# Kernel optimization log

Measured on AMD Instinct MI355X. Metric: run time of the kernel, lower is better.

Reference implementation:

```python
import jax, jax.numpy as jnp
import numpy as np

B, T, D, H, E = 4, 2048, 1024, 2048, 8
TOP_K = int(E * 0.25)  # = 2


def setup_inputs() -> dict:
    key = jax.random.key(0)
    ks = jax.random.split(key, 6)
    x = jax.random.normal(ks[0], (B, T, D), dtype=jnp.float32)
    gate = jax.random.normal(ks[1], (D, E), dtype=jnp.float32)
    # per-expert 2-layer MLP params (D -> H -> D), stacked over experts
    W1 = jax.random.normal(ks[2], (E, D, H), dtype=jnp.float32) * (D ** -0.5)
    b1 = jnp.zeros((E, H), dtype=jnp.float32)
    W2 = jax.random.normal(ks[3], (E, H, D), dtype=jnp.float32) * (H ** -0.5)
    b2 = jnp.zeros((E, D), dtype=jnp.float32)
    return {"x": x, "gate": gate, "W1": W1, "b1": b1, "W2": W2, "b2": b2}


def reference(x, gate, W1, b1, W2, b2):
    # gating: softmax over experts, then top-k mask, renormalize (L1 over experts)
    raw_gate = jax.nn.softmax(jnp.einsum('btd,de->bte', x, gate), axis=-1)  # [B,T,E]
    topk_scores, topk_idx = jax.lax.top_k(raw_gate, TOP_K)                   # [B,T,k]
    mask = jax.nn.one_hot(topk_idx, E, dtype=raw_gate.dtype).sum(axis=-2)    # [B,T,E]
    gate_topk = mask * raw_gate
    gate_topk = gate_topk / jnp.maximum(gate_topk.sum(axis=-1, keepdims=True), 1e-12)
    # dense all-expert compute (faithful to the original: every expert sees every token)
    h = jax.nn.relu(jnp.einsum('btd,edh->beth', x, W1) + b1[None, :, None, :])  # [B,E,T,H]
    expert_out = jnp.einsum('beth,ehd->betd', h, W2) + b2[None, :, None, :]     # [B,E,T,D]
    # weighted combine
    out = jnp.einsum('bte,betd->btd', gate_topk, expert_out)  # [B,T,D]
    return out
```

## Files before the change

### kernel.cpp

```cpp
#include <hip/hip_runtime.h>

#define E_      8
#define D_      1024
#define H_      2048
#define TOKENS  8192
#define RROWS   16384
#define HPAD_ROWS (RROWS + 128)

using bf16x8 = __attribute__((ext_vector_type(8))) __bf16;
using f32x4  = __attribute__((ext_vector_type(4))) float;

__device__ __forceinline__ unsigned short f2bf(float f) {
  unsigned u = __builtin_bit_cast(unsigned, f);
  u += 0x7fffu + ((u >> 16) & 1u);
  return (unsigned short)(u >> 16);
}
__device__ __forceinline__ float bf2f(unsigned short u) {
  unsigned v = (unsigned)u << 16;
  return __builtin_bit_cast(float, v);
}

#define GLDS16(g, l) __builtin_amdgcn_global_load_lds( \
    (const __attribute__((address_space(1))) unsigned int*)(g), \
    (__attribute__((address_space(3))) unsigned int*)(l), 16, 0, 0)

#define SBAR() asm volatile("s_barrier" ::: "memory")


__global__ void transpose_cvt_kernel(const float* __restrict__ src,
                                     unsigned short* __restrict__ dst,
                                     int R, int C) {
  int tilesC = C >> 6, tilesR = R >> 6;
  int per = tilesR * tilesC;
  int b = blockIdx.x;
  int e = b / per, rem = b % per;
  int rb = rem / tilesC, cb = rem % tilesC;
  __shared__ float tile[64][65];
  const float* s = src + (size_t)e * R * C;
  unsigned short* d = dst + (size_t)e * R * C;
  int r0 = rb << 6, c0 = cb << 6;
#pragma unroll
  for (int i = 0; i < 16; i++) {
    int idx = threadIdx.x + i * 256;
    int lr = idx >> 6, lc = idx & 63;
    tile[lr][lc] = s[(size_t)(r0 + lr) * C + (c0 + lc)];
  }
  __syncthreads();
#pragma unroll
  for (int i = 0; i < 16; i++) {
    int idx = threadIdx.x + i * 256;
    int lr = idx >> 6, lc = idx & 63;
    d[(size_t)(c0 + lr) * R + (r0 + lc)] = f2bf(tile[lc][lr]);
  }
}

__global__ void gating_kernel(const float* __restrict__ x, const float* __restrict__ gate,
                              unsigned short* __restrict__ xb,
                              int* __restrict__ sel, float* __restrict__ wsel) {
  int lane = threadIdx.x & 63, wid = threadIdx.x >> 6;
  int t = (blockIdx.x << 2) + wid;
  const float* xr = x + (size_t)t * D_;
  unsigned short* xbr = xb + (size_t)t * D_;
  float acc[8];
#pragma unroll
  for (int e = 0; e < 8; e++) acc[e] = 0.f;
#pragma unroll
  for (int i = 0; i < 4; i++) {
    int d0 = (i << 8) + (lane << 2);
    float4 xv = *reinterpret_cast<const float4*>(xr + d0);
    ushort4 o = make_ushort4(f2bf(xv.x), f2bf(xv.y), f2bf(xv.z), f2bf(xv.w));
    *reinterpret_cast<ushort4*>(xbr + d0) = o;
    float xa[4] = {xv.x, xv.y, xv.z, xv.w};
#pragma unroll
    for (int j = 0; j < 4; j++) {
      const float4* g4 = reinterpret_cast<const float4*>(gate + (size_t)(d0 + j) * 8);
      float4 ga = g4[0], gb = g4[1];
      acc[0] += xa[j] * ga.x; acc[1] += xa[j] * ga.y;
      acc[2] += xa[j] * ga.z; acc[3] += xa[j] * ga.w;
      acc[4] += xa[j] * gb.x; acc[5] += xa[j] * gb.y;
      acc[6] += xa[j] * gb.z; acc[7] += xa[j] * gb.w;
    }
  }
#pragma unroll
  for (int e = 0; e < 8; e++) {
#pragma unroll
    for (int off = 32; off; off >>= 1) acc[e] += __shfl_xor(acc[e], off);
  }
  if (lane == 0) {
    int i0 = 0; float v0 = acc[0];
#pragma unroll
    for (int e = 1; e < 8; e++) if (acc[e] > v0) { v0 = acc[e]; i0 = e; }
    int i1 = -1; float v1 = -3.4e38f;
#pragma unroll
    for (int e = 0; e < 8; e++) if (e != i0 && acc[e] > v1) { v1 = acc[e]; i1 = e; }
    float p1 = expf(v1 - v0);
    float inv = 1.f / (1.f + p1);
    sel[t * 2] = i0; sel[t * 2 + 1] = i1;
    wsel[t * 2] = inv; wsel[t * 2 + 1] = p1 * inv;
  }
}

__global__ __launch_bounds__(1024) void route_kernel(
    const int* __restrict__ sel, int* __restrict__ cnt, int* __restrict__ off,
    int* __restrict__ tok_id, int* __restrict__ pos) {
  const int tid = threadIdx.x;
  const int lane = tid & 63, wid = tid >> 6;
  __shared__ int wtot[16][8];
  __shared__ int woff[16][8];
  __shared__ int offs[8];
  int sv[16];
  const int s0 = tid << 4;
#pragma unroll
  for (int q = 0; q < 4; q++) {
    int4 v = reinterpret_cast<const int4*>(sel + s0)[q];
    sv[q * 4 + 0] = v.x; sv[q * 4 + 1] = v.y;
    sv[q * 4 + 2] = v.z; sv[q * 4 + 3] = v.w;
  }
  int h[8];
#pragma unroll
  for (int e = 0; e < 8; e++) h[e] = 0;
#pragma unroll
  for (int j = 0; j < 16; j++) {
    int ev = sv[j];
#pragma unroll
    for (int e = 0; e < 8; e++) h[e] += (ev == e) ? 1 : 0;
  }
  int excl[8];
#pragma unroll
  for (int e = 0; e < 8; e++) {
    int v = h[e];
#pragma unroll
    for (int d = 1; d < 64; d <<= 1) {
      int u = __shfl_up(v, d);
      if (lane >= d) v += u;
    }
    excl[e] = v - h[e];
    if (lane == 63) wtot[wid][e] = v;
  }
  __syncthreads();
  if (tid == 0) {
    int run[8];
#pragma unroll
    for (int e = 0; e < 8; e++) run[e] = 0;
    for (int w = 0; w < 16; w++)
#pragma unroll
      for (int e = 0; e < 8; e++) { woff[w][e] = run[e]; run[e] += wtot[w][e]; }
    int a = 0;
    for (int e = 0; e < 8; e++) { offs[e] = a; off[e] = a; cnt[e] = run[e]; a += run[e]; }
  }
  __syncthreads();
  int base[8];
#pragma unroll
  for (int e = 0; e < 8; e++) base[e] = offs[e] + woff[wid][e] + excl[e];
#pragma unroll
  for (int j = 0; j < 16; j++) {
    int ev = sv[j];
    int p = 0;
#pragma unroll
    for (int e = 0; e < 8; e++) if (ev == e) { p = base[e]; base[e] = p + 1; }
    pos[s0 + j] = p;
    tok_id[p] = (s0 + j) >> 1;
  }
}


#define STAGE_T(slot, kh) do { \
  const size_t ko = (size_t)(kh) << 7; \
  _Pragma("unroll") \
  for (int i = 0; i < 4; i++) { \
    GLDS16(Ab + gA[i] + ko, &Asm[slot][((wid << 2) + i) << 9]); \
    GLDS16(Bb + gB[i] + ko, &Bsm[slot][((wid << 2) + i) << 9]); \
  } \
} while (0)

__global__ __launch_bounds__(256, 2) void gemm1_kernel(
    const unsigned short* __restrict__ xb,
    const unsigned short* __restrict__ w1t,
    const float* __restrict__ b1,
    unsigned short* __restrict__ hbuf,
    const int* __restrict__ tok_id,
    const int* __restrict__ cnt, const int* __restrict__ off) {
  const int nwg = E_ * 64 * 16;
  const int raw = blockIdx.x;
  const int bid = (raw & 7) * (nwg >> 3) + (raw >> 3);
  const int e  = bid >> 10;
  const int rb = (bid >> 4) & 63;
  const int cb = bid & 15;
  const int rows = cnt[e];
  const int m0 = rb << 7;
  if (m0 >= rows) return;
  const int base = off[e];
  const int tid = threadIdx.x, lane = tid & 63, wid = tid >> 6;
  const int wr = wid >> 1, wc = wid & 1;

  __shared__ __align__(16) unsigned short Asm[2][128 * 64];
  __shared__ __align__(16) unsigned short Bsm[2][128 * 64];

  const int c8 = lane & 7, r8 = lane >> 3;
  const size_t swz = (size_t)((c8 ^ r8) << 4);
  size_t gA[4], gB[4];
  const int n0 = cb << 7;
#pragma unroll
  for (int i = 0; i < 4; i++) {
    int r = ((wid << 2) + i) << 3;
    int ar = m0 + r + r8; if (ar >= rows) ar = rows - 1;
    gA[i] = (size_t)tok_id[base + ar] * (D_ * 2) + swz;
    gB[i] = (size_t)(n0 + r + r8) * (D_ * 2) + swz;
  }
  const char* Ab = (const char*)xb;
  const char* Bb = (const char*)w1t + (size_t)e * H_ * D_ * 2;

  const int aRow = ((wr << 6) + (lane & 15)) * 128;
  const int bRow = ((wc << 6) + (lane & 15)) * 128;
  const int cby0 = (((lane >> 4)) ^ (lane & 7)) << 4;
  const int cby1 = ((4 + (lane >> 4)) ^ (lane & 7)) << 4;

  f32x4 acc[4][4] = {};
  const int KH = D_ / 64;

  STAGE_T(0, 0);
  STAGE_T(1, 1);
  asm volatile("s_waitcnt vmcnt(8)" ::: "memory");
  SBAR();

  for (int kh = 0; kh < KH; ++kh) {
    const int cur = kh & 1;
    const char* Ap = (const char*)&Asm[cur][0] + aRow;
    const char* Bp = (const char*)&Bsm[cur][0] + bRow;
    bf16x8 a[4], b[4], a2[4], b2[4];
#pragma unroll
    for (int m = 0; m < 4; m++) a[m]  = *(const bf16x8*)(Ap + cby0 + m * 2048);
#pragma unroll
    for (int n = 0; n < 4; n++) b[n]  = *(const bf16x8*)(Bp + cby0 + n * 2048);
#pragma unroll
    for (int m = 0; m < 4; m++) a2[m] = *(const bf16x8*)(Ap + cby1 + m * 2048);
#pragma unroll
    for (int n = 0; n < 4; n++) b2[n] = *(const bf16x8*)(Bp + cby1 + n * 2048);
    asm volatile("s_waitcnt lgkmcnt(0)" ::: "memory");
    __builtin_amdgcn_sched_barrier(0);
    SBAR();
    if (kh + 2 < KH) STAGE_T(cur, kh + 2);
    __builtin_amdgcn_s_setprio(1);
#pragma unroll
    for (int m = 0; m < 4; m++)
#pragma unroll
      for (int n = 0; n < 4; n++)
        acc[m][n] = __builtin_amdgcn_mfma_f32_16x16x32_bf16(a[m], b[n], acc[m][n], 0, 0, 0);
#pragma unroll
    for (int m = 0; m < 4; m++)
#pragma unroll
      for (int n = 0; n < 4; n++)
        acc[m][n] = __builtin_amdgcn_mfma_f32_16x16x32_bf16(a2[m], b2[n], acc[m][n], 0, 0, 0);
    __builtin_amdgcn_s_setprio(0);
    if (kh + 2 < KH) {
      asm volatile("s_waitcnt vmcnt(8)" ::: "memory");
    } else if (kh + 1 < KH) {
      asm volatile("s_waitcnt vmcnt(0)" ::: "memory");
    }
    SBAR();
  }

  const int rcnt = rows - m0;
  const float* b1e = b1 + e * H_;
#pragma unroll
  for (int m = 0; m < 4; m++) {
#pragma unroll
    for (int q = 0; q < 4; q++) {
      int rl = (wr << 6) + (m << 4) + ((lane >> 4) << 2) + q;
      if (rl < rcnt) {
        unsigned short* hrow = hbuf + (size_t)(base + m0 + rl) * H_;
#pragma unroll
        for (int n = 0; n < 4; n++) {
          int ncol = n0 + (wc << 6) + (n << 4) + (lane & 15);
          float v = acc[m][n][q] + b1e[ncol];
          hrow[ncol] = f2bf(fmaxf(v, 0.f));
        }
      }
    }
  }
}

__global__ __launch_bounds__(256, 2) void gemm2_kernel(
    const unsigned short* __restrict__ hbuf,
    const unsigned short* __restrict__ w2t,
    unsigned short* __restrict__ eout,
    const int* __restrict__ cnt, const int* __restrict__ off) {
  const int nwg = E_ * 64 * 8;
  const int raw = blockIdx.x;
  const int bid = (raw & 7) * (nwg >> 3) + (raw >> 3);
  const int e  = bid >> 9;
  const int rb = (bid >> 3) & 63;
  const int cb = bid & 7;
  const int rows = cnt[e];
  const int m0 = rb << 7;
  if (m0 >= rows) return;
  const int base = off[e];
  const int tid = threadIdx.x, lane = tid & 63, wid = tid >> 6;
  const int wr = wid >> 1, wc = wid & 1;

  __shared__ __align__(16) unsigned short Asm[2][128 * 64];
  __shared__ __align__(16) unsigned short Bsm[2][128 * 64];

  const int c8 = lane & 7, r8 = lane >> 3;
  const size_t swz = (size_t)((c8 ^ r8) << 4);
  size_t gA[4], gB[4];
  const int n0 = cb << 7;
#pragma unroll
  for (int i = 0; i < 4; i++) {
    int r = ((wid << 2) + i) << 3;
    gA[i] = (size_t)(base + m0 + r + r8) * (H_ * 2) + swz;
    gB[i] = (size_t)(n0 + r + r8) * (H_ * 2) + swz;
  }
  const char* Ab = (const char*)hbuf;
  const char* Bb = (const char*)w2t + (size_t)e * D_ * H_ * 2;

  const int aRow = ((wr << 6) + (lane & 15)) * 128;
  const int bRow = ((wc << 6) + (lane & 15)) * 128;
  const int cby0 = (((lane >> 4)) ^ (lane & 7)) << 4;
  const int cby1 = ((4 + (lane >> 4)) ^ (lane & 7)) << 4;

  f32x4 acc[4][4] = {};
  const int KH = H_ / 64;

  STAGE_T(0, 0);
  STAGE_T(1, 1);
  asm volatile("s_waitcnt vmcnt(8)" ::: "memory");
  SBAR();

  for (int kh = 0; kh < KH; ++kh) {
    const int cur = kh & 1;
    const char* Ap = (const char*)&Asm[cur][0] + aRow;
    const char* Bp = (const char*)&Bsm[cur][0] + bRow;
    bf16x8 a[4], b[4], a2[4], b2[4];
#pragma unroll
    for (int m = 0; m < 4; m++) a[m]  = *(const bf16x8*)(Ap + cby0 + m * 2048);
#pragma unroll
    for (int n = 0; n < 4; n++) b[n]  = *(const bf16x8*)(Bp + cby0 + n * 2048);
#pragma unroll
    for (int m = 0; m < 4; m++) a2[m] = *(const bf16x8*)(Ap + cby1 + m * 2048);
#pragma unroll
    for (int n = 0; n < 4; n++) b2[n] = *(const bf16x8*)(Bp + cby1 + n * 2048);
    asm volatile("s_waitcnt lgkmcnt(0)" ::: "memory");
    __builtin_amdgcn_sched_barrier(0);
    SBAR();
    if (kh + 2 < KH) STAGE_T(cur, kh + 2);
    __builtin_amdgcn_s_setprio(1);
#pragma unroll
    for (int m = 0; m < 4; m++)
#pragma unroll
      for (int n = 0; n < 4; n++)
        acc[m][n] = __builtin_amdgcn_mfma_f32_16x16x32_bf16(a[m], b[n], acc[m][n], 0, 0, 0);
#pragma unroll
    for (int m = 0; m < 4; m++)
#pragma unroll
      for (int n = 0; n < 4; n++)
        acc[m][n] = __builtin_amdgcn_mfma_f32_16x16x32_bf16(a2[m], b2[n], acc[m][n], 0, 0, 0);
    __builtin_amdgcn_s_setprio(0);
    if (kh + 2 < KH) {
      asm volatile("s_waitcnt vmcnt(8)" ::: "memory");
    } else if (kh + 1 < KH) {
      asm volatile("s_waitcnt vmcnt(0)" ::: "memory");
    }
    SBAR();
  }

  const int rcnt = rows - m0;
#pragma unroll
  for (int m = 0; m < 4; m++) {
#pragma unroll
    for (int q = 0; q < 4; q++) {
      int rl = (wr << 6) + (m << 4) + ((lane >> 4) << 2) + q;
      if (rl < rcnt) {
        unsigned short* erow = eout + (size_t)(base + m0 + rl) * D_;
#pragma unroll
        for (int n = 0; n < 4; n++) {
          int ncol = n0 + (wc << 6) + (n << 4) + (lane & 15);
          erow[ncol] = f2bf(acc[m][n][q]);
        }
      }
    }
  }
}

__global__ void combine_kernel(const unsigned short* __restrict__ eout,
                               const float* __restrict__ b2,
                               const int* __restrict__ sel, const float* __restrict__ wsel,
                               const int* __restrict__ pos,
                               float* __restrict__ out) {
  int t = blockIdx.x;
  int d = threadIdx.x << 2;
  int e0 = sel[t * 2], e1 = sel[t * 2 + 1];
  float w0 = wsel[t * 2], w1 = wsel[t * 2 + 1];
  int p0 = pos[t * 2], p1 = pos[t * 2 + 1];
  ushort4 y0 = *reinterpret_cast<const ushort4*>(eout + (size_t)p0 * D_ + d);
  ushort4 y1 = *reinterpret_cast<const ushort4*>(eout + (size_t)p1 * D_ + d);
  float4 c0 = *reinterpret_cast<const float4*>(b2 + (size_t)e0 * D_ + d);
  float4 c1 = *reinterpret_cast<const float4*>(b2 + (size_t)e1 * D_ + d);
  float4 o;
  o.x = w0 * (bf2f(y0.x) + c0.x) + w1 * (bf2f(y1.x) + c1.x);
  o.y = w0 * (bf2f(y0.y) + c0.y) + w1 * (bf2f(y1.y) + c1.y);
  o.z = w0 * (bf2f(y0.z) + c0.z) + w1 * (bf2f(y1.z) + c1.z);
  o.w = w0 * (bf2f(y0.w) + c0.w) + w1 * (bf2f(y1.w) + c1.w);
  *reinterpret_cast<float4*>(out + (size_t)t * D_ + d) = o;
}


extern "C" void kernel_launch(void* const* d_in, const int* in_sizes, int n_in,
                              void* d_out, int out_size, void* d_ws, size_t ws_size,
                              hipStream_t stream) {
  (void)in_sizes; (void)n_in; (void)ws_size; (void)out_size;
  const float* x    = (const float*)d_in[0];
  const float* gate = (const float*)d_in[1];
  const float* W1   = (const float*)d_in[2];
  const float* b1   = (const float*)d_in[3];
  const float* W2   = (const float*)d_in[4];
  const float* b2   = (const float*)d_in[5];
  float* out = (float*)d_out;

  char* p = (char*)d_ws;
  unsigned short* xb   = (unsigned short*)p; p += (size_t)TOKENS * D_ * 2;
  unsigned short* w1t  = (unsigned short*)p; p += (size_t)E_ * H_ * D_ * 2;
  unsigned short* w2t  = (unsigned short*)p; p += (size_t)E_ * D_ * H_ * 2;
  unsigned short* hbuf = (unsigned short*)p; p += (size_t)HPAD_ROWS * H_ * 2;
  int*   tok  = (int*)p;   p += (size_t)RROWS * 4;
  int*   pos  = (int*)p;   p += (size_t)TOKENS * 2 * 4;
  int*   sel  = (int*)p;   p += (size_t)TOKENS * 2 * 4;
  float* wsel = (float*)p; p += (size_t)TOKENS * 2 * 4;
  int* cnt    = (int*)p;   p += 32 * 4;
  int* off    = (int*)p;   p += 32 * 4;
  unsigned short* eout = w1t;

  transpose_cvt_kernel<<<E_ * (D_ / 64) * (H_ / 64), 256, 0, stream>>>(W1, w1t, D_, H_);
  transpose_cvt_kernel<<<E_ * (H_ / 64) * (D_ / 64), 256, 0, stream>>>(W2, w2t, H_, D_);
  gating_kernel<<<TOKENS / 4, 256, 0, stream>>>(x, gate, xb, sel, wsel);
  route_kernel<<<1, 1024, 0, stream>>>(sel, cnt, off, tok, pos);
  gemm1_kernel<<<E_ * 64 * 16, 256, 0, stream>>>(xb, w1t, b1, hbuf, tok, cnt, off);
  gemm2_kernel<<<E_ * 64 * 8, 256, 0, stream>>>(hbuf, w2t, eout, cnt, off);
  combine_kernel<<<TOKENS, 256, 0, stream>>>(eout, b2, sel, wsel, pos, out);
}
```

Before: 299.1 us.

## Enlarge grouped GEMM tiles to 256x256 with 512-thread workgroups

Both expert GEMMs move from 128x128 output tiles with 4 waves to 256x256 tiles with 8 waves. Each wave now holds a 128x64 accumulator block and interleaves the two half-K MFMA passes with LDS fragment loads. The goal is more reuse per byte staged into LDS and fewer workgroups. In exchange it uses 128KB of LDS per block and many more accumulator registers, and it adds padding waste on ragged per-expert row counts, which is why the hbuf padding is increased.

```diff
diff --git a/kernel.cpp b/kernel.cpp
--- a/kernel.cpp
+++ b/kernel.cpp
@@ -5,7 +5,7 @@
 #define H_      2048
 #define TOKENS  8192
 #define RROWS   16384
-#define HPAD_ROWS (RROWS + 128)
+#define HPAD_ROWS (RROWS + 256)
 
 using bf16x8 = __attribute__((ext_vector_type(8))) __bf16;
 using f32x4  = __attribute__((ext_vector_type(4))) float;
@@ -164,126 +164,21 @@
 }
 
 
-#define STAGE_T(slot, kh) do { \
+#define STAGE256(slot, kh) do { \
   const size_t ko = (size_t)(kh) << 7; \
   _Pragma("unroll") \
   for (int i = 0; i < 4; i++) { \
-    GLDS16(Ab + gA[i] + ko, &Asm[slot][((wid << 2) + i) << 9]); \
-    GLDS16(Bb + gB[i] + ko, &Bsm[slot][((wid << 2) + i) << 9]); \
+    GLDS16(Ab + aO[i] + ko, (char*)&Asm[slot][0] + (i << 13) + (wid << 10)); \
+    GLDS16(Bb + bO[i] + ko, (char*)&Bsm[slot][0] + (i << 13) + (wid << 10)); \
   } \
 } while (0)
 
-__global__ __launch_bounds__(256, 2) void gemm1_kernel(
+__global__ __launch_bounds__(512, 2) void gemm1_kernel(
     const unsigned short* __restrict__ xb,
     const unsigned short* __restrict__ w1t,
     const float* __restrict__ b1,
     unsigned short* __restrict__ hbuf,
     const int* __restrict__ tok_id,
-    const int* __restrict__ cnt, const int* __restrict__ off) {
-  const int nwg = E_ * 64 * 16;
-  const int raw = blockIdx.x;
-  const int bid = (raw & 7) * (nwg >> 3) + (raw >> 3);
-  const int e  = bid >> 10;
-  const int rb = (bid >> 4) & 63;
-  const int cb = bid & 15;
-  const int rows = cnt[e];
-  const int m0 = rb << 7;
-  if (m0 >= rows) return;
-  const int base = off[e];
-  const int tid = threadIdx.x, lane = tid & 63, wid = tid >> 6;
-  const int wr = wid >> 1, wc = wid & 1;
-
-  __shared__ __align__(16) unsigned short Asm[2][128 * 64];
-  __shared__ __align__(16) unsigned short Bsm[2][128 * 64];
-
-  const int c8 = lane & 7, r8 = lane >> 3;
-  const size_t swz = (size_t)((c8 ^ r8) << 4);
-  size_t gA[4], gB[4];
-  const int n0 = cb << 7;
-#pragma unroll
-  for (int i = 0; i < 4; i++) {
-    int r = ((wid << 2) + i) << 3;
-    int ar = m0 + r + r8; if (ar >= rows) ar = rows - 1;
-    gA[i] = (size_t)tok_id[base + ar] * (D_ * 2) + swz;
-    gB[i] = (size_t)(n0 + r + r8) * (D_ * 2) + swz;
-  }
-  const char* Ab = (const char*)xb;
-  const char* Bb = (const char*)w1t + (size_t)e * H_ * D_ * 2;
-
-  const int aRow = ((wr << 6) + (lane & 15)) * 128;
-  const int bRow = ((wc << 6) + (lane & 15)) * 128;
-  const int cby0 = (((lane >> 4)) ^ (lane & 7)) << 4;
-  const int cby1 = ((4 + (lane >> 4)) ^ (lane & 7)) << 4;
-
-  f32x4 acc[4][4] = {};
-  const int KH = D_ / 64;
-
-  STAGE_T(0, 0);
-  STAGE_T(1, 1);
-  asm volatile("s_waitcnt vmcnt(8)" ::: "memory");
-  SBAR();
-
-  for (int kh = 0; kh < KH; ++kh) {
-    const int cur = kh & 1;
-    const char* Ap = (const char*)&Asm[cur][0] + aRow;
-    const char* Bp = (const char*)&Bsm[cur][0] + bRow;
-    bf16x8 a[4], b[4], a2[4], b2[4];
-#pragma unroll
-    for (int m = 0; m < 4; m++) a[m]  = *(const bf16x8*)(Ap + cby0 + m * 2048);
-#pragma unroll
-    for (int n = 0; n < 4; n++) b[n]  = *(const bf16x8*)(Bp + cby0 + n * 2048);
-#pragma unroll
-    for (int m = 0; m < 4; m++) a2[m] = *(const bf16x8*)(Ap + cby1 + m * 2048);
-#pragma unroll
-    for (int n = 0; n < 4; n++) b2[n] = *(const bf16x8*)(Bp + cby1 + n * 2048);
-    asm volatile("s_waitcnt lgkmcnt(0)" ::: "memory");
-    __builtin_amdgcn_sched_barrier(0);
-    SBAR();
-    if (kh + 2 < KH) STAGE_T(cur, kh + 2);
-    __builtin_amdgcn_s_setprio(1);
-#pragma unroll
-    for (int m = 0; m < 4; m++)
-#pragma unroll
-      for (int n = 0; n < 4; n++)
-        acc[m][n] = __builtin_amdgcn_mfma_f32_16x16x32_bf16(a[m], b[n], acc[m][n], 0, 0, 0);
-#pragma unroll
-    for (int m = 0; m < 4; m++)
-#pragma unroll
-      for (int n = 0; n < 4; n++)
-        acc[m][n] = __builtin_amdgcn_mfma_f32_16x16x32_bf16(a2[m], b2[n], acc[m][n], 0, 0, 0);
-    __builtin_amdgcn_s_setprio(0);
-    if (kh + 2 < KH) {
-      asm volatile("s_waitcnt vmcnt(8)" ::: "memory");
-    } else if (kh + 1 < KH) {
-      asm volatile("s_waitcnt vmcnt(0)" ::: "memory");
-    }
-    SBAR();
-  }
-
-  const int rcnt = rows - m0;
-  const float* b1e = b1 + e * H_;
-#pragma unroll
-  for (int m = 0; m < 4; m++) {
-#pragma unroll
-    for (int q = 0; q < 4; q++) {
-      int rl = (wr << 6) + (m << 4) + ((lane >> 4) << 2) + q;
-      if (rl < rcnt) {
-        unsigned short* hrow = hbuf + (size_t)(base + m0 + rl) * H_;
-#pragma unroll
-        for (int n = 0; n < 4; n++) {
-          int ncol = n0 + (wc << 6) + (n << 4) + (lane & 15);
-          float v = acc[m][n][q] + b1e[ncol];
-          hrow[ncol] = f2bf(fmaxf(v, 0.f));
-        }
-      }
-    }
-  }
-}
-
-__global__ __launch_bounds__(256, 2) void gemm2_kernel(
-    const unsigned short* __restrict__ hbuf,
-    const unsigned short* __restrict__ w2t,
-    unsigned short* __restrict__ eout,
     const int* __restrict__ cnt, const int* __restrict__ off) {
   const int nwg = E_ * 64 * 8;
   const int raw = blockIdx.x;
@@ -292,38 +187,39 @@
   const int rb = (bid >> 3) & 63;
   const int cb = bid & 7;
   const int rows = cnt[e];
-  const int m0 = rb << 7;
+  const int m0 = rb << 8;
   if (m0 >= rows) return;
   const int base = off[e];
   const int tid = threadIdx.x, lane = tid & 63, wid = tid >> 6;
-  const int wr = wid >> 1, wc = wid & 1;
-
-  __shared__ __align__(16) unsigned short Asm[2][128 * 64];
-  __shared__ __align__(16) unsigned short Bsm[2][128 * 64];
-
-  const int c8 = lane & 7, r8 = lane >> 3;
-  const size_t swz = (size_t)((c8 ^ r8) << 4);
-  size_t gA[4], gB[4];
-  const int n0 = cb << 7;
+  const int wr = wid >> 2, wc = wid & 3;
+
+  __shared__ __align__(16) unsigned short Asm[2][256 * 64];
+  __shared__ __align__(16) unsigned short Bsm[2][256 * 64];
+
+  const size_t swz = (size_t)(((tid & 7) ^ ((tid >> 3) & 7)) << 4);
+  const int srow = tid >> 3;
+  const int n0 = cb << 8;
+  size_t aO[4], bO[4];
+  const char* Ab = (const char*)xb;
+  const char* Bb = (const char*)w1t + (size_t)e * H_ * D_ * 2;
 #pragma unroll
   for (int i = 0; i < 4; i++) {
-    int r = ((wid << 2) + i) << 3;
-    gA[i] = (size_t)(base + m0 + r + r8) * (H_ * 2) + swz;
-    gB[i] = (size_t)(n0 + r + r8) * (H_ * 2) + swz;
-  }
-  const char* Ab = (const char*)hbuf;
-  const char* Bb = (const char*)w2t + (size_t)e * D_ * H_ * 2;
-
-  const int aRow = ((wr << 6) + (lane & 15)) * 128;
+    int r = (i << 6) + srow;
+    int ar = m0 + r; if (ar >= rows) ar = rows - 1;
+    aO[i] = (size_t)tok_id[base + ar] * (D_ * 2) + swz;
+    bO[i] = (size_t)(n0 + r) * (D_ * 2) + swz;
+  }
+
+  const int aRow = ((wr << 7) + (lane & 15)) * 128;
   const int bRow = ((wc << 6) + (lane & 15)) * 128;
   const int cby0 = (((lane >> 4)) ^ (lane & 7)) << 4;
   const int cby1 = ((4 + (lane >> 4)) ^ (lane & 7)) << 4;
 
-  f32x4 acc[4][4] = {};
-  const int KH = H_ / 64;
-
-  STAGE_T(0, 0);
-  STAGE_T(1, 1);
+  f32x4 acc[8][4] = {};
+  const int KH = D_ / 64;
+
+  STAGE256(0, 0);
+  STAGE256(1, 1);
   asm volatile("s_waitcnt vmcnt(8)" ::: "memory");
   SBAR();
 
@@ -331,30 +227,32 @@
     const int cur = kh & 1;
     const char* Ap = (const char*)&Asm[cur][0] + aRow;
     const char* Bp = (const char*)&Bsm[cur][0] + bRow;
-    bf16x8 a[4], b[4], a2[4], b2[4];
-#pragma unroll
-    for (int m = 0; m < 4; m++) a[m]  = *(const bf16x8*)(Ap + cby0 + m * 2048);
-#pragma unroll
-    for (int n = 0; n < 4; n++) b[n]  = *(const bf16x8*)(Bp + cby0 + n * 2048);
-#pragma unroll
-    for (int m = 0; m < 4; m++) a2[m] = *(const bf16x8*)(Ap + cby1 + m * 2048);
-#pragma unroll
-    for (int n = 0; n < 4; n++) b2[n] = *(const bf16x8*)(Bp + cby1 + n * 2048);
+    bf16x8 a[8], b[4];
+#pragma unroll
+    for (int m = 0; m < 8; m++) a[m] = *(const bf16x8*)(Ap + cby0 + m * 2048);
+#pragma unroll
+    for (int n = 0; n < 4; n++) b[n] = *(const bf16x8*)(Bp + cby0 + n * 2048);
+    __builtin_amdgcn_s_setprio(1);
+#pragma unroll
+    for (int m = 0; m < 8; m++)
+#pragma unroll
+      for (int n = 0; n < 4; n++)
+        acc[m][n] = __builtin_amdgcn_mfma_f32_16x16x32_bf16(a[m], b[n], acc[m][n], 0, 0, 0);
+    __builtin_amdgcn_s_setprio(0);
+#pragma unroll
+    for (int m = 0; m < 8; m++) a[m] = *(const bf16x8*)(Ap + cby1 + m * 2048);
+#pragma unroll
+    for (int n = 0; n < 4; n++) b[n] = *(const bf16x8*)(Bp + cby1 + n * 2048);
     asm volatile("s_waitcnt lgkmcnt(0)" ::: "memory");
     __builtin_amdgcn_sched_barrier(0);
     SBAR();
-    if (kh + 2 < KH) STAGE_T(cur, kh + 2);
+    if (kh + 2 < KH) STAGE256(cur, kh + 2);
     __builtin_amdgcn_s_setprio(1);
 #pragma unroll
-    for (int m = 0; m < 4; m++)
+    for (int m = 0; m < 8; m++)
 #pragma unroll
       for (int n = 0; n < 4; n++)
         acc[m][n] = __builtin_amdgcn_mfma_f32_16x16x32_bf16(a[m], b[n], acc[m][n], 0, 0, 0);
-#pragma unroll
-    for (int m = 0; m < 4; m++)
-#pragma unroll
-      for (int n = 0; n < 4; n++)
-        acc[m][n] = __builtin_amdgcn_mfma_f32_16x16x32_bf16(a2[m], b2[n], acc[m][n], 0, 0, 0);
     __builtin_amdgcn_s_setprio(0);
     if (kh + 2 < KH) {
       asm volatile("s_waitcnt vmcnt(8)" ::: "memory");
@@ -365,11 +263,117 @@
   }
 
   const int rcnt = rows - m0;
-#pragma unroll
-  for (int m = 0; m < 4; m++) {
+  const float* b1e = b1 + e * H_;
+#pragma unroll
+  for (int m = 0; m < 8; m++) {
 #pragma unroll
     for (int q = 0; q < 4; q++) {
-      int rl = (wr << 6) + (m << 4) + ((lane >> 4) << 2) + q;
+      int rl = (wr << 7) + (m << 4) + ((lane >> 4) << 2) + q;
+      if (rl < rcnt) {
+        unsigned short* hrow = hbuf + (size_t)(base + m0 + rl) * H_;
+#pragma unroll
+        for (int n = 0; n < 4; n++) {
+          int ncol = n0 + (wc << 6) + (n << 4) + (lane & 15);
+          float v = acc[m][n][q] + b1e[ncol];
+          hrow[ncol] = f2bf(fmaxf(v, 0.f));
+        }
+      }
+    }
+  }
+}
+
+__global__ __launch_bounds__(512, 2) void gemm2_kernel(
+    const unsigned short* __restrict__ hbuf,
+    const unsigned short* __restrict__ w2t,
+    unsigned short* __restrict__ eout,
+    const int* __restrict__ cnt, const int* __restrict__ off) {
+  const int nwg = E_ * 64 * 4;
+  const int raw = blockIdx.x;
+  const int bid = (raw & 7) * (nwg >> 3) + (raw >> 3);
+  const int e  = bid >> 8;
+  const int rb = (bid >> 2) & 63;
+  const int cb = bid & 3;
+  const int rows = cnt[e];
+  const int m0 = rb << 8;
+  if (m0 >= rows) return;
+  const int base = off[e];
+  const int tid = threadIdx.x, lane = tid & 63, wid = tid >> 6;
+  const int wr = wid >> 2, wc = wid & 3;
+
+  __shared__ __align__(16) unsigned short Asm[2][256 * 64];
+  __shared__ __align__(16) unsigned short Bsm[2][256 * 64];
+
+  const size_t swz = (size_t)(((tid & 7) ^ ((tid >> 3) & 7)) << 4);
+  const int srow = tid >> 3;
+  const int n0 = cb << 8;
+  size_t aO[4], bO[4];
+  const char* Ab = (const char*)hbuf;
+  const char* Bb = (const char*)w2t + (size_t)e * D_ * H_ * 2;
+#pragma unroll
+  for (int i = 0; i < 4; i++) {
+    int r = (i << 6) + srow;
+    aO[i] = (size_t)(base + m0 + r) * (H_ * 2) + swz;
+    bO[i] = (size_t)(n0 + r) * (H_ * 2) + swz;
+  }
+
+  const int aRow = ((wr << 7) + (lane & 15)) * 128;
+  const int bRow = ((wc << 6) + (lane & 15)) * 128;
+  const int cby0 = (((lane >> 4)) ^ (lane & 7)) << 4;
+  const int cby1 = ((4 + (lane >> 4)) ^ (lane & 7)) << 4;
+
+  f32x4 acc[8][4] = {};
+  const int KH = H_ / 64;
+
+  STAGE256(0, 0);
+  STAGE256(1, 1);
+  asm volatile("s_waitcnt vmcnt(8)" ::: "memory");
+  SBAR();
+
+  for (int kh = 0; kh < KH; ++kh) {
+    const int cur = kh & 1;
+    const char* Ap = (const char*)&Asm[cur][0] + aRow;
+    const char* Bp = (const char*)&Bsm[cur][0] + bRow;
+    bf16x8 a[8], b[4];
+#pragma unroll
+    for (int m = 0; m < 8; m++) a[m] = *(const bf16x8*)(Ap + cby0 + m * 2048);
+#pragma unroll
+    for (int n = 0; n < 4; n++) b[n] = *(const bf16x8*)(Bp + cby0 + n * 2048);
+    __builtin_amdgcn_s_setprio(1);
+#pragma unroll
+    for (int m = 0; m < 8; m++)
+#pragma unroll
+      for (int n = 0; n < 4; n++)
+        acc[m][n] = __builtin_amdgcn_mfma_f32_16x16x32_bf16(a[m], b[n], acc[m][n], 0, 0, 0);
+    __builtin_amdgcn_s_setprio(0);
+#pragma unroll
+    for (int m = 0; m < 8; m++) a[m] = *(const bf16x8*)(Ap + cby1 + m * 2048);
+#pragma unroll
+    for (int n = 0; n < 4; n++) b[n] = *(const bf16x8*)(Bp + cby1 + n * 2048);
+    asm volatile("s_waitcnt lgkmcnt(0)" ::: "memory");
+    __builtin_amdgcn_sched_barrier(0);
+    SBAR();
+    if (kh + 2 < KH) STAGE256(cur, kh + 2);
+    __builtin_amdgcn_s_setprio(1);
+#pragma unroll
+    for (int m = 0; m < 8; m++)
+#pragma unroll
+      for (int n = 0; n < 4; n++)
+        acc[m][n] = __builtin_amdgcn_mfma_f32_16x16x32_bf16(a[m], b[n], acc[m][n], 0, 0, 0);
+    __builtin_amdgcn_s_setprio(0);
+    if (kh + 2 < KH) {
+      asm volatile("s_waitcnt vmcnt(8)" ::: "memory");
+    } else if (kh + 1 < KH) {
+      asm volatile("s_waitcnt vmcnt(0)" ::: "memory");
+    }
+    SBAR();
+  }
+
+  const int rcnt = rows - m0;
+#pragma unroll
+  for (int m = 0; m < 8; m++) {
+#pragma unroll
+    for (int q = 0; q < 4; q++) {
+      int rl = (wr << 7) + (m << 4) + ((lane >> 4) << 2) + q;
       if (rl < rcnt) {
         unsigned short* erow = eout + (size_t)(base + m0 + rl) * D_;
 #pragma unroll
@@ -434,7 +438,7 @@
   transpose_cvt_kernel<<<E_ * (H_ / 64) * (D_ / 64), 256, 0, stream>>>(W2, w2t, H_, D_);
   gating_kernel<<<TOKENS / 4, 256, 0, stream>>>(x, gate, xb, sel, wsel);
   route_kernel<<<1, 1024, 0, stream>>>(sel, cnt, off, tok, pos);
-  gemm1_kernel<<<E_ * 64 * 16, 256, 0, stream>>>(xb, w1t, b1, hbuf, tok, cnt, off);
-  gemm2_kernel<<<E_ * 64 * 8, 256, 0, stream>>>(hbuf, w2t, eout, cnt, off);
+  gemm1_kernel<<<E_ * 64 * 8, 512, 0, stream>>>(xb, w1t, b1, hbuf, tok, cnt, off);
+  gemm2_kernel<<<E_ * 64 * 4, 512, 0, stream>>>(hbuf, w2t, eout, cnt, off);
   combine_kernel<<<TOKENS, 256, 0, stream>>>(eout, b2, sel, wsel, pos, out);
 }
```

After: 327.6 us. 9.5% more time.
